# Kernel tuning notes

Measured on AMD Instinct MI355X. Metric: run time of the kernel, lower is better.

## Reference

```python
import jax, jax.numpy as jnp
import numpy as np

DIM = 768
N_HEADS = 12
HEAD_DIM = DIM // N_HEADS
MLP_DIM = 3072
DEPTH = 12
B, N = 16, 512


def setup_inputs() -> dict:
    key = jax.random.key(0)
    ks = jax.random.split(key, 12)
    s = 0.02
    return {
        "x": jax.random.normal(ks[0], (B, N, DIM), dtype=jnp.float32),
        "ln_w": jnp.ones((DIM,), jnp.float32),
        "ln_b": jnp.zeros((DIM,), jnp.float32),
        "wq": jax.random.normal(ks[1], (DIM, DIM), jnp.float32) * s,
        "bq": jnp.zeros((DIM,), jnp.float32),
        "wk": jax.random.normal(ks[2], (DIM, DIM), jnp.float32) * s,
        "bk": jnp.zeros((DIM,), jnp.float32),
        "wv": jax.random.normal(ks[3], (DIM, DIM), jnp.float32) * s,
        "bv": jnp.zeros((DIM,), jnp.float32),
        "w1": jax.random.normal(ks[4], (DIM, MLP_DIM), jnp.float32) * s,
        "b1": jnp.zeros((MLP_DIM,), jnp.float32),
        "w2": jax.random.normal(ks[5], (MLP_DIM, DIM), jnp.float32) * s,
        "b2": jnp.zeros((DIM,), jnp.float32),
    }


def _layernorm(x, w, b):
    mu = jnp.mean(x, axis=-1, keepdims=True)
    var = jnp.var(x, axis=-1, keepdims=True)
    return (x - mu) * jax.lax.rsqrt(var + 1e-5) * w + b


def _mha(x, wq, bq, wk, bk, wv, bv):
    # x: [b, n, dim]; weights stored as [in, out]
    def heads(t):
        return t.reshape(B, N, N_HEADS, HEAD_DIM).transpose(0, 2, 1, 3)  # b h n d
    q = heads(x @ wq + bq)
    k = heads(x @ wk + bk)
    v = heads(x @ wv + bv)
    scores = jnp.einsum('bhqd,bhkd->bhqk', q, k) / np.sqrt(HEAD_DIM).astype(np.float32)
    attn = jax.nn.softmax(scores, axis=-1)
    o = jnp.einsum('bhqk,bhkd->bhqd', attn, v)
    return o.transpose(0, 2, 1, 3).reshape(B, N, DIM)


def reference(x, ln_w, ln_b, wq, bq, wk, bk, wv, bv, w1, b1, w2, b2):
    # Dropout is identity in eval mode. Same weights reused each depth iteration.
    for _ in range(DEPTH):
        x = _mha(_layernorm(x, ln_w, ln_b), wq, bq, wk, bk, wv, bv) + x
        h = _layernorm(x, ln_w, ln_b)
        h = jax.nn.gelu(h @ w1 + b1, approximate=False) @ w2 + b2
        x = h + x
    return x
```

## Files before the change

### kernel.cpp

```cpp
#include <hip/hip_runtime.h>

typedef __bf16 bf16x8 __attribute__((ext_vector_type(8)));
typedef float f32x4 __attribute__((ext_vector_type(4)));
typedef unsigned short ushort8_t __attribute__((ext_vector_type(8)));
typedef unsigned short ushort4_t __attribute__((ext_vector_type(4)));

#define MFMA16(a, b, c) __builtin_amdgcn_mfma_f32_16x16x32_bf16((a), (b), (c), 0, 0, 0)

#define GLOAD16(gp, lp)                                                        \
  __builtin_amdgcn_global_load_lds(                                            \
      (__attribute__((address_space(1))) void*)(gp),                           \
      (__attribute__((address_space(3))) void*)(lp), 16, 0, 0)

#define WAITVM(N) asm volatile("s_waitcnt vmcnt(" #N ")" ::: "memory")
#define SCHEDFENCE __builtin_amdgcn_sched_barrier(0)

__device__ __forceinline__ unsigned short f2bf(float f) {
  unsigned u = __builtin_bit_cast(unsigned, f);
  return (unsigned short)((u + 0x7FFFu + ((u >> 16) & 1u)) >> 16);
}


__global__ __launch_bounds__(256) void transpose_f2b_tiled(
    const float* __restrict__ src, unsigned short* __restrict__ dst,
    int Kdim, int Ndim) {
  const long u = (long)blockIdx.x * 256 + threadIdx.x;
  const long total = ((long)Kdim * Ndim) >> 3;
  if (u >= total) return;
  const int kt32 = Kdim >> 5;
  const long tile = u >> 6;
  const int t8 = (int)(u & 63);
  const int chunk = t8 >> 4, rowlow = t8 & 15;
  const int n = (int)(tile / kt32) * 16 + rowlow;
  const int k0 = (int)(tile % kt32) * 32 + chunk * 8;
  ushort8_t o;
#pragma unroll
  for (int e = 0; e < 8; e++) o[e] = f2bf(src[(long)(k0 + e) * Ndim + n]);
  *(ushort8_t*)(dst + (u << 3)) = o;
}

__global__ __launch_bounds__(256) void ln_kernel(
    const float* __restrict__ x, const float* __restrict__ gw,
    const float* __restrict__ gb, unsigned short* __restrict__ h) {
  const int row = blockIdx.x * 4 + (threadIdx.x >> 6);
  const int l = threadIdx.x & 63;
  const float* xr = x + (long)row * 768;
  f32x4 va[3];
#pragma unroll
  for (int i = 0; i < 3; i++) va[i] = *(const f32x4*)(xr + i * 256 + l * 4);
  float s = 0.f, ss = 0.f;
#pragma unroll
  for (int i = 0; i < 3; i++)
#pragma unroll
    for (int j = 0; j < 4; j++) {
      float t = va[i][j];
      s += t;
      ss += t * t;
    }
#pragma unroll
  for (int off = 1; off < 64; off <<= 1) {
    s += __shfl_xor(s, off, 64);
    ss += __shfl_xor(ss, off, 64);
  }
  const float mu = s * (1.f / 768.f);
  const float var = ss * (1.f / 768.f) - mu * mu;
  const float inv = rsqrtf(var + 1e-5f);
  const long tb = ((long)(row >> 4) * 24) << 9;
  const int rlow = (row & 15) * 8;
  const int coff = ((l >> 1) & 3) * 128 + rlow + (l & 1) * 4;
#pragma unroll
  for (int i = 0; i < 3; i++) {
    f32x4 wv = *(const f32x4*)(gw + i * 256 + l * 4);
    f32x4 bv = *(const f32x4*)(gb + i * 256 + l * 4);
    ushort4_t o;
#pragma unroll
    for (int j = 0; j < 4; j++) o[j] = f2bf((va[i][j] - mu) * inv * wv[j] + bv[j]);
    const long addr = tb + ((long)(i * 8 + (l >> 3)) << 9) + coff;
    *(ushort4_t*)(h + addr) = o;
  }
}

enum { EPI_QKV = 0, EPI_GELU = 1, EPI_RES = 2 };

template <int EPI>
__global__ __launch_bounds__(512) void gemm256p(
    const unsigned short* __restrict__ A, const unsigned short* __restrict__ BT,
    int K, const float* __restrict__ bb0, unsigned short* __restrict__ o0) {
  __shared__ unsigned short As[2][2][8192];
  __shared__ unsigned short Bs[2][2][8192];
  const int tid = threadIdx.x;
  const int w = tid >> 6, l = tid & 63;
  const int lr = l & 15, lg = l >> 4;
  const int wr = w >> 2, wc = w & 3;

  const int nx = gridDim.x;
  const int nwg = nx * gridDim.y;
  int wg = blockIdx.y * nx + blockIdx.x;
  {
    const int qq = nwg >> 3, rr = nwg & 7;
    const int xcd = wg & 7, idx = wg >> 3;
    wg = (xcd < rr ? xcd * (qq + 1) : rr * (qq + 1) + (xcd - rr) * qq) + idx;
  }
  const int bx = wg % nx, by = wg / nx;
  const int m0 = by * 256, n0 = bx * 256;

  const int nk32 = K >> 5;
  const long abase = (long)(m0 >> 4) * nk32;
  const long bbase = (long)(n0 >> 4) * nk32;

  auto stage = [&](int t) {
    const int slot = t & 1;
#pragma unroll
    for (int kk = 0; kk < 2; kk++) {
      const int pk = t * 2 + kk;
      GLOAD16(A + ((abase + (long)w * nk32 + pk) << 9) + l * 8,
              &As[slot][kk][w * 512 + l * 8]);
      GLOAD16(A + ((abase + (long)(w + 8) * nk32 + pk) << 9) + l * 8,
              &As[slot][kk][(w + 8) * 512 + l * 8]);
      GLOAD16(BT + ((bbase + (long)w * nk32 + pk) << 9) + l * 8,
              &Bs[slot][kk][w * 512 + l * 8]);
      GLOAD16(BT + ((bbase + (long)(w + 8) * nk32 + pk) << 9) + l * 8,
              &Bs[slot][kk][(w + 8) * 512 + l * 8]);
    }
  };

  f32x4 acc[8][4] = {};
  const int nk = K >> 6;
  stage(0);
  stage(1);
  for (int t = 0; t < nk; ++t) {
    const int slot = t & 1;
    if (t + 1 < nk) { WAITVM(8); } else { WAITVM(0); }
    SCHEDFENCE;
    __builtin_amdgcn_s_barrier();
    SCHEDFENCE;
#pragma unroll
    for (int kk = 0; kk < 2; kk++) {
      bf16x8 a[8], b[4];
#pragma unroll
      for (int i = 0; i < 8; i++)
        a[i] = *(const bf16x8*)(&As[slot][kk][(wr * 8 + i) * 512 + l * 8]);
#pragma unroll
      for (int j = 0; j < 4; j++)
        b[j] = *(const bf16x8*)(&Bs[slot][kk][(wc * 4 + j) * 512 + l * 8]);
      __builtin_amdgcn_s_setprio(1);
#pragma unroll
      for (int i = 0; i < 8; i++)
#pragma unroll
        for (int j = 0; j < 4; j++) acc[i][j] = MFMA16(a[i], b[j], acc[i][j]);
      __builtin_amdgcn_s_setprio(0);
    }
    SCHEDFENCE;
    __builtin_amdgcn_s_barrier();
    SCHEDFENCE;
    if (t + 2 < nk) stage(t + 2);
  }

#pragma unroll
  for (int fm = 0; fm < 8; fm++) {
    const int r = m0 + wr * 128 + fm * 16 + lg * 4;
#pragma unroll
    for (int fn = 0; fn < 4; fn++) {
      const int c = n0 + wc * 64 + fn * 16 + lr;
      const float bv = bb0[c];
      const long cpart = ((long)(c >> 5) << 9) + ((c >> 3) & 3) * 128 + (c & 7);
#pragma unroll
      for (int q = 0; q < 4; q++) {
        const int row = r + q;
        float v = acc[fm][fn][q] + bv;
        const float u = v * (0.7978845608f + 0.0356774081f * v * v);
        const float g = v / (1.0f + __expf(-2.0f * u));
        o0[(((long)(row >> 4) * 96) << 9) + cpart + (row & 15) * 8] = f2bf(g);
      }
    }
  }
}

template <int EPI, int MREP>
__global__ __launch_bounds__(256) void gemm_bt(
    const unsigned short* __restrict__ A, const unsigned short* __restrict__ BT,
    int K, const float* __restrict__ bb0, const float* __restrict__ bb1,
    const float* __restrict__ bb2, unsigned short* __restrict__ o0,
    unsigned short* __restrict__ o1, unsigned short* __restrict__ o2,
    const float* oFin, float* oFout) {
  constexpr int BM = MREP * 32;
  constexpr int AG = BM / 16;
  __shared__ unsigned short As[2][2][AG * 512];
  __shared__ unsigned short Bs[2][2][8 * 512];
  const int tid = threadIdx.x;
  const int w = tid >> 6, l = tid & 63;
  const int lr = l & 15, lg = l >> 4;
  const int wr = w >> 1, wc = w & 1;

  const int nx = gridDim.x;
  const int nwg = nx * gridDim.y;
  int wg = blockIdx.y * nx + blockIdx.x;
  {
    const int qq = nwg >> 3, rr = nwg & 7;
    const int xcd = wg & 7, idx = wg >> 3;
    wg = (xcd < rr ? xcd * (qq + 1) : rr * (qq + 1) + (xcd - rr) * qq) + idx;
  }
  const int bx = wg % nx, by = wg / nx;
  const int m0 = by * BM, n0 = bx * 128;

  const int nk32 = K >> 5;
  const long abase = (long)(m0 >> 4) * nk32;
  const long bbase = (long)(n0 >> 4) * nk32;

  auto stage = [&](int buf, int kt) {
#pragma unroll
    for (int kk = 0; kk < 2; kk++) {
      const int pk = kt * 2 + kk;
#pragma unroll
      for (int t = 0; t < AG / 4; t++) {
        const int g = w + t * 4;
        GLOAD16(A + ((abase + (long)g * nk32 + pk) << 9) + l * 8,
                &As[buf][kk][g * 512 + l * 8]);
      }
#pragma unroll
      for (int t = 0; t < 2; t++) {
        const int g = w + t * 4;
        GLOAD16(BT + ((bbase + (long)g * nk32 + pk) << 9) + l * 8,
                &Bs[buf][kk][g * 512 + l * 8]);
      }
    }
  };

  f32x4 acc[MREP][4] = {};
  const int nk = K >> 6;
  stage(0, 0);
  for (int kt = 0; kt < nk; ++kt) {
    const int cur = kt & 1;
    __syncthreads();
    if (kt + 1 < nk) stage(cur ^ 1, kt + 1);
#pragma unroll
    for (int kk = 0; kk < 2; kk++) {
      bf16x8 a[MREP], b[4];
#pragma unroll
      for (int i = 0; i < MREP; i++)
        a[i] = *(const bf16x8*)(&As[cur][kk][(wr * MREP + i) * 512 + l * 8]);
#pragma unroll
      for (int j = 0; j < 4; j++)
        b[j] = *(const bf16x8*)(&Bs[cur][kk][(wc * 4 + j) * 512 + l * 8]);
      __builtin_amdgcn_s_setprio(1);
#pragma unroll
      for (int i = 0; i < MREP; i++)
#pragma unroll
        for (int j = 0; j < 4; j++) acc[i][j] = MFMA16(a[i], b[j], acc[i][j]);
      __builtin_amdgcn_s_setprio(0);
    }
  }

  if (EPI == EPI_QKV) {
    const int whichq = n0 / 768;
    const int cc0 = n0 - whichq * 768;
    const float* bias = whichq == 0 ? bb0 : whichq == 1 ? bb1 : bb2;
    if (whichq < 2) {
      unsigned short* dst = whichq == 0 ? o0 : o1;
#pragma unroll
      for (int i = 0; i < MREP; i++) {
        const int r = m0 + wr * MREP * 16 + i * 16 + lg * 4;
#pragma unroll
        for (int j = 0; j < 4; j++) {
          const int ccol = cc0 + wc * 64 + j * 16 + lr;
          const int hd = ccol >> 6, d = ccol & 63;
          const float bv = bias[ccol];
#pragma unroll
          for (int q = 0; q < 4; q++) {
            const int row = r + q;
            const int bidx = row >> 9, n = row & 511;
            const long addr = ((long)(bidx * 12 + hd) * 512 + n) * 64 + d;
            dst[addr] = f2bf(acc[i][j][q] + bv);
          }
        }
      }
    } else {
#pragma unroll
      for (int i = 0; i < MREP; i++) {
        const int r = m0 + wr * MREP * 16 + i * 16 + lg * 4;
        const int bidx = r >> 9, nb = r & 511;
#pragma unroll
        for (int j = 0; j < 4; j++) {
          const int ccol = cc0 + wc * 64 + j * 16 + lr;
          const int hd = ccol >> 6, d = ccol & 63;
          const float bv = bias[ccol];
          ushort4_t pk;
#pragma unroll
          for (int q = 0; q < 4; q++) pk[q] = f2bf(acc[i][j][q] + bv);
          *(ushort4_t*)(&o2[((long)(bidx * 12 + hd) * 64 + d) * 512 + nb]) = pk;
        }
      }
    }
  } else if (EPI == EPI_GELU) {
#pragma unroll
    for (int i = 0; i < MREP; i++) {
      const int r = m0 + wr * MREP * 16 + i * 16 + lg * 4;
#pragma unroll
      for (int j = 0; j < 4; j++) {
        const int c = n0 + wc * 64 + j * 16 + lr;
        const float bv = bb0[c];
        const long cpart = ((long)(c >> 5) << 9) + ((c >> 3) & 3) * 128 + (c & 7);
#pragma unroll
        for (int q = 0; q < 4; q++) {
          const int row = r + q;
          float v = acc[i][j][q] + bv;
          const float u = v * (0.7978845608f + 0.0356774081f * v * v);
          const float g = v / (1.0f + __expf(-2.0f * u));
          o0[(((long)(row >> 4) * 96) << 9) + cpart + (row & 15) * 8] = f2bf(g);
        }
      }
    }
  } else {
#pragma unroll
    for (int i = 0; i < MREP; i++) {
      const int r = m0 + wr * MREP * 16 + i * 16 + lg * 4;
#pragma unroll
      for (int j = 0; j < 4; j++) {
        const int c = n0 + wc * 64 + j * 16 + lr;
        const float bv = bb0[c];
#pragma unroll
        for (int q = 0; q < 4; q++) {
          const long addr = (long)(r + q) * 768 + c;
          oFout[addr] = acc[i][j][q] + bv + oFin[addr];
        }
      }
    }
  }
}

__global__ __launch_bounds__(256) void attn_kernel(
    const unsigned short* __restrict__ qg, const unsigned short* __restrict__ kg,
    const unsigned short* __restrict__ vtg, float* __restrict__ x) {
  __shared__ unsigned short Sh[128 * 64];
  __shared__ unsigned short Ks[2][64 * 64];
  __shared__ unsigned short Vt[2][64 * 64];
  const int qt = blockIdx.x, h = blockIdx.y, b = blockIdx.z;
  const int bh = b * 12 + h;
  const int tid = threadIdx.x, w = tid >> 6, l = tid & 63;
  const int lr = l & 15, lg = l >> 4;
  const int fchunk = ((l & 7) ^ ((l >> 3) & 7)) * 8;
  const int rk = lr & 7;

  const unsigned short* qbase =
      qg + ((long)bh * 512 + qt * 128 + w * 32 + (l >> 3)) * 64 + fchunk;
  unsigned short* shW = &Sh[w * 2048 + l * 8];
#pragma unroll
  for (int cc = 0; cc < 4; cc++) GLOAD16(qbase + cc * 8 * 64, shW + cc * 512);

  const unsigned short* kbase =
      kg + ((long)bh * 512 + w * 16 + (l >> 3)) * 64 + fchunk;
  const unsigned short* vbase =
      vtg + ((long)bh * 64 + w * 16 + (l >> 3)) * 512 + fchunk;
  unsigned short* KsW = &Ks[0][w * 1024 + l * 8];
  unsigned short* VtW = &Vt[0][w * 1024 + l * 8];

  auto stageKV = [&](int buf, int kt) {
#pragma unroll
    for (int cc = 0; cc < 2; cc++) {
      GLOAD16(kbase + (kt * 64 + cc * 8) * 64, KsW + buf * 4096 + cc * 512);
      GLOAD16(vbase + cc * 8 * 512 + kt * 64, VtW + buf * 4096 + cc * 512);
    }
  };
  stageKV(0, 0);
  __syncthreads();

  bf16x8 qa[2][2];
#pragma unroll
  for (int mi = 0; mi < 2; mi++)
#pragma unroll
    for (int ds = 0; ds < 2; ds++) {
      qa[mi][ds] = *(const bf16x8*)(&Sh[(w * 32 + mi * 16 + lr) * 64 +
                                        ((ds * 4 + lg) ^ rk) * 8]);
#pragma unroll
      for (int e = 0; e < 8; e++)
        qa[mi][ds][e] = (__bf16)(0.125f * (float)qa[mi][ds][e]);
    }

  unsigned short* Pw = &Sh[w * 2048];
  float lsum[8] = {};
  f32x4 o[2][4] = {};

  for (int kt = 0; kt < 8; ++kt) {
    const int cur = kt & 1;
    if (kt < 7) stageKV(cur ^ 1, kt + 1);

    f32x4 s[2][4] = {};
#pragma unroll
    for (int ds = 0; ds < 2; ++ds) {
      bf16x8 kb[4];
#pragma unroll
      for (int nj = 0; nj < 4; nj++)
        kb[nj] = *(const bf16x8*)(&Ks[cur][(nj * 16 + lr) * 64 +
                                           ((ds * 4 + lg) ^ rk) * 8]);
#pragma unroll
      for (int mi = 0; mi < 2; mi++)
#pragma unroll
        for (int nj = 0; nj < 4; nj++) s[mi][nj] = MFMA16(qa[mi][ds], kb[nj], s[mi][nj]);
    }

#pragma unroll
    for (int mi = 0; mi < 2; mi++)
#pragma unroll
      for (int nj = 0; nj < 4; nj++) {
        const int cL = nj * 2 + (lr >> 3);
#pragma unroll
        for (int q = 0; q < 4; q++) {
          const int row = mi * 16 + lg * 4 + q;
          const float p = __expf(s[mi][nj][q]);
          lsum[mi * 4 + q] += p;
          Pw[row * 64 + ((cL ^ (row & 7)) * 8) + (lr & 7)] = f2bf(p);
        }
      }

#pragma unroll
    for (int ks = 0; ks < 2; ++ks) {
      bf16x8 pa[2], vb[4];
#pragma unroll
      for (int mi = 0; mi < 2; mi++)
        pa[mi] = *(const bf16x8*)(&Pw[(mi * 16 + lr) * 64 +
                                      ((ks * 4 + lg) ^ rk) * 8]);
#pragma unroll
      for (int dj = 0; dj < 4; dj++)
        vb[dj] = *(const bf16x8*)(&Vt[cur][(dj * 16 + lr) * 64 +
                                           ((ks * 4 + lg) ^ rk) * 8]);
#pragma unroll
      for (int mi = 0; mi < 2; mi++)
#pragma unroll
        for (int dj = 0; dj < 4; dj++) o[mi][dj] = MFMA16(pa[mi], vb[dj], o[mi][dj]);
    }
    __syncthreads();
  }

#pragma unroll
  for (int i = 0; i < 8; i++) {
#pragma unroll
    for (int off = 1; off < 16; off <<= 1) lsum[i] += __shfl_xor(lsum[i], off, 64);
  }

#pragma unroll
  for (int mi = 0; mi < 2; mi++) {
#pragma unroll
    for (int q = 0; q < 4; q++) {
      const int n = qt * 128 + w * 32 + mi * 16 + lg * 4 + q;
      const float inv = 1.0f / lsum[mi * 4 + q];
      const long base = ((long)(b * 512 + n)) * 768 + h * 64;
#pragma unroll
      for (int dj = 0; dj < 4; dj++) {
        const long a = base + dj * 16 + lr;
        x[a] = x[a] + o[mi][dj][q] * inv;
      }
    }
  }
}

extern "C" void kernel_launch(void* const* d_in, const int* in_sizes, int n_in,
                              void* d_out, int out_size, void* d_ws,
                              size_t ws_size, hipStream_t stream) {
  const float* x_in = (const float*)d_in[0];
  const float* ln_w = (const float*)d_in[1];
  const float* ln_b = (const float*)d_in[2];
  const float* wq = (const float*)d_in[3];
  const float* bq = (const float*)d_in[4];
  const float* wk = (const float*)d_in[5];
  const float* bk = (const float*)d_in[6];
  const float* wv = (const float*)d_in[7];
  const float* bv = (const float*)d_in[8];
  const float* w1 = (const float*)d_in[9];
  const float* b1 = (const float*)d_in[10];
  const float* w2 = (const float*)d_in[11];
  const float* b2 = (const float*)d_in[12];

  char* p = (char*)d_ws;
  float* xw = (float*)p;            p += 8192L * 768 * 4;
  unsigned short* hbuf = (unsigned short*)p;  p += 8192L * 768 * 2;
  unsigned short* wqkvT = (unsigned short*)p; p += 2304L * 768 * 2;
  unsigned short* w1T = (unsigned short*)p;   p += 3072L * 768 * 2;
  unsigned short* w2T = (unsigned short*)p;   p += 768L * 3072 * 2;
  unsigned short* qb = (unsigned short*)p;
  unsigned short* kb = qb + 6291456L;
  unsigned short* vt = kb + 6291456L;
  unsigned short* gbuf = qb;

  hipMemcpyAsync(xw, x_in, 8192L * 768 * 4, hipMemcpyDeviceToDevice, stream);

  transpose_f2b_tiled<<<(768 * 768 / 8 + 255) / 256, 256, 0, stream>>>(
      wq, wqkvT, 768, 768);
  transpose_f2b_tiled<<<(768 * 768 / 8 + 255) / 256, 256, 0, stream>>>(
      wk, wqkvT + 768L * 768, 768, 768);
  transpose_f2b_tiled<<<(768 * 768 / 8 + 255) / 256, 256, 0, stream>>>(
      wv, wqkvT + 2L * 768 * 768, 768, 768);
  transpose_f2b_tiled<<<(768 * 3072 / 8 + 255) / 256, 256, 0, stream>>>(
      w1, w1T, 768, 3072);
  transpose_f2b_tiled<<<(768 * 3072 / 8 + 255) / 256, 256, 0, stream>>>(
      w2, w2T, 3072, 768);

  for (int layer = 0; layer < 12; ++layer) {
    ln_kernel<<<2048, 256, 0, stream>>>(xw, ln_w, ln_b, hbuf);
    gemm_bt<EPI_QKV, 4><<<dim3(18, 64), 256, 0, stream>>>(
        hbuf, wqkvT, 768, bq, bk, bv, qb, kb, vt, nullptr, nullptr);
    attn_kernel<<<dim3(4, 12, 16), 256, 0, stream>>>(qb, kb, vt, xw);
    ln_kernel<<<2048, 256, 0, stream>>>(xw, ln_w, ln_b, hbuf);
    gemm256p<EPI_GELU><<<dim3(12, 32), 512, 0, stream>>>(
        hbuf, w1T, 768, b1, gbuf);
    gemm_bt<EPI_RES, 2><<<dim3(6, 128), 256, 0, stream>>>(
        gbuf, w2T, 3072, b2, nullptr, nullptr, nullptr, nullptr, nullptr, xw,
        layer == 11 ? (float*)d_out : xw);
  }
}
```

Before: 2.596 ms.

## Split MLP-up GEMM into four quarter-tile phases with finer-grained LDS staging

Rewrites the 256x256 GELU GEMM so each 64-wide K step is processed as four quadrant sub-phases over A and B half-tiles. LDS is reorganised into four slots holding half-tiles, and global-to-LDS loads for the next halves are issued between the phases. This interleaves memory traffic with MFMA work and reduces register pressure from fragment loads (4 A fragments instead of 8). The cost is four barriers per K step instead of two, plus a more intricate slot-reuse schedule that must avoid overwrite races.

```diff
diff --git a/kernel.cpp b/kernel.cpp
--- a/kernel.cpp
+++ b/kernel.cpp
@@ -13,6 +13,7 @@
       (__attribute__((address_space(3))) void*)(lp), 16, 0, 0)
 
 #define WAITVM(N) asm volatile("s_waitcnt vmcnt(" #N ")" ::: "memory")
+#define WAITLGKM asm volatile("s_waitcnt lgkmcnt(0)" ::: "memory")
 #define SCHEDFENCE __builtin_amdgcn_sched_barrier(0)
 
 __device__ __forceinline__ unsigned short f2bf(float f) {
@@ -82,12 +83,11 @@
 
 enum { EPI_QKV = 0, EPI_GELU = 1, EPI_RES = 2 };
 
-template <int EPI>
-__global__ __launch_bounds__(512) void gemm256p(
+__global__ __launch_bounds__(512) void gemm256f(
     const unsigned short* __restrict__ A, const unsigned short* __restrict__ BT,
     int K, const float* __restrict__ bb0, unsigned short* __restrict__ o0) {
-  __shared__ unsigned short As[2][2][8192];
-  __shared__ unsigned short Bs[2][2][8192];
+  __shared__ unsigned short Asl[4][16 * 512];
+  __shared__ unsigned short Bsl[4][16 * 512];
   const int tid = threadIdx.x;
   const int w = tid >> 6, l = tid & 63;
   const int lr = l & 15, lg = l >> 4;
@@ -108,52 +108,111 @@
   const long abase = (long)(m0 >> 4) * nk32;
   const long bbase = (long)(n0 >> 4) * nk32;
 
-  auto stage = [&](int t) {
-    const int slot = t & 1;
-#pragma unroll
-    for (int kk = 0; kk < 2; kk++) {
-      const int pk = t * 2 + kk;
-      GLOAD16(A + ((abase + (long)w * nk32 + pk) << 9) + l * 8,
-              &As[slot][kk][w * 512 + l * 8]);
-      GLOAD16(A + ((abase + (long)(w + 8) * nk32 + pk) << 9) + l * 8,
-              &As[slot][kk][(w + 8) * 512 + l * 8]);
-      GLOAD16(BT + ((bbase + (long)w * nk32 + pk) << 9) + l * 8,
-              &Bs[slot][kk][w * 512 + l * 8]);
-      GLOAD16(BT + ((bbase + (long)(w + 8) * nk32 + pk) << 9) + l * 8,
-              &Bs[slot][kk][(w + 8) * 512 + l * 8]);
-    }
+  auto stageA = [&](int t, int mh) {
+    const int slot = (2 * t + mh) & 3;
+    const int G = (w >> 2) * 8 + mh * 4 + (w & 3);
+    const int loff = ((w >> 2) * 8 + (w & 3) * 2) * 512;
+#pragma unroll
+    for (int kk = 0; kk < 2; kk++)
+      GLOAD16(A + ((abase + (long)G * nk32 + t * 2 + kk) << 9) + l * 8,
+              &Asl[slot][loff + kk * 512 + l * 8]);
+  };
+  auto stageB = [&](int t, int nh) {
+    const int slot = (2 * t + nh) & 3;
+    const int G = (w >> 1) * 4 + nh * 2 + (w & 1);
+    const int loff = (((w >> 1) * 2 + (w & 1)) * 2) * 512;
+#pragma unroll
+    for (int kk = 0; kk < 2; kk++)
+      GLOAD16(BT + ((bbase + (long)G * nk32 + t * 2 + kk) << 9) + l * 8,
+              &Bsl[slot][loff + kk * 512 + l * 8]);
   };
 
   f32x4 acc[8][4] = {};
   const int nk = K >> 6;
-  stage(0);
-  stage(1);
+
+  stageA(0, 0); stageB(0, 0); stageB(0, 1); stageA(0, 1);
+  stageA(1, 0); stageB(1, 0); stageB(1, 1);
+
   for (int t = 0; t < nk; ++t) {
-    const int slot = t & 1;
-    if (t + 1 < nk) { WAITVM(8); } else { WAITVM(0); }
+    const int sA0 = (2 * t) & 3, sA1 = (2 * t + 1) & 3;
+    if (t < nk - 1) { WAITVM(6); } else { WAITVM(0); }
     SCHEDFENCE;
     __builtin_amdgcn_s_barrier();
     SCHEDFENCE;
-#pragma unroll
-    for (int kk = 0; kk < 2; kk++) {
-      bf16x8 a[8], b[4];
-#pragma unroll
-      for (int i = 0; i < 8; i++)
-        a[i] = *(const bf16x8*)(&As[slot][kk][(wr * 8 + i) * 512 + l * 8]);
-#pragma unroll
-      for (int j = 0; j < 4; j++)
-        b[j] = *(const bf16x8*)(&Bs[slot][kk][(wc * 4 + j) * 512 + l * 8]);
-      __builtin_amdgcn_s_setprio(1);
-#pragma unroll
-      for (int i = 0; i < 8; i++)
-#pragma unroll
-        for (int j = 0; j < 4; j++) acc[i][j] = MFMA16(a[i], b[j], acc[i][j]);
-      __builtin_amdgcn_s_setprio(0);
-    }
+
+    bf16x8 a[4][2], b0[2][2], b1[2][2];
+
+#pragma unroll
+    for (int f = 0; f < 4; f++)
+#pragma unroll
+      for (int kk = 0; kk < 2; kk++)
+        a[f][kk] = *(const bf16x8*)&Asl[sA0][((wr * 4 + f) * 2 + kk) * 512 + l * 8];
+#pragma unroll
+    for (int g2 = 0; g2 < 2; g2++)
+#pragma unroll
+      for (int kk = 0; kk < 2; kk++)
+        b0[g2][kk] = *(const bf16x8*)&Bsl[sA0][((wc * 2 + g2) * 2 + kk) * 512 + l * 8];
+    if (t + 1 < nk) stageA(t + 1, 1);
+    WAITLGKM; SCHEDFENCE;
+    __builtin_amdgcn_s_barrier(); SCHEDFENCE;
+    __builtin_amdgcn_s_setprio(1);
+#pragma unroll
+    for (int f = 0; f < 4; f++)
+#pragma unroll
+      for (int g2 = 0; g2 < 2; g2++)
+#pragma unroll
+        for (int kk = 0; kk < 2; kk++)
+          acc[f][g2] = MFMA16(a[f][kk], b0[g2][kk], acc[f][g2]);
+    __builtin_amdgcn_s_setprio(0);
+
+#pragma unroll
+    for (int g2 = 0; g2 < 2; g2++)
+#pragma unroll
+      for (int kk = 0; kk < 2; kk++)
+        b1[g2][kk] = *(const bf16x8*)&Bsl[sA1][((wc * 2 + g2) * 2 + kk) * 512 + l * 8];
+    if (t + 2 < nk) stageA(t + 2, 0);
+    WAITLGKM; SCHEDFENCE;
+    __builtin_amdgcn_s_barrier(); SCHEDFENCE;
+    __builtin_amdgcn_s_setprio(1);
+#pragma unroll
+    for (int f = 0; f < 4; f++)
+#pragma unroll
+      for (int g2 = 0; g2 < 2; g2++)
+#pragma unroll
+        for (int kk = 0; kk < 2; kk++)
+          acc[f][2 + g2] = MFMA16(a[f][kk], b1[g2][kk], acc[f][2 + g2]);
+    __builtin_amdgcn_s_setprio(0);
+
+#pragma unroll
+    for (int f = 0; f < 4; f++)
+#pragma unroll
+      for (int kk = 0; kk < 2; kk++)
+        a[f][kk] = *(const bf16x8*)&Asl[sA1][((wr * 4 + f) * 2 + kk) * 512 + l * 8];
+    if (t + 2 < nk) stageB(t + 2, 0);
+    WAITLGKM; SCHEDFENCE;
+    __builtin_amdgcn_s_barrier(); SCHEDFENCE;
+    __builtin_amdgcn_s_setprio(1);
+#pragma unroll
+    for (int f = 0; f < 4; f++)
+#pragma unroll
+      for (int g2 = 0; g2 < 2; g2++)
+#pragma unroll
+        for (int kk = 0; kk < 2; kk++)
+          acc[4 + f][2 + g2] = MFMA16(a[f][kk], b1[g2][kk], acc[4 + f][2 + g2]);
+    __builtin_amdgcn_s_setprio(0);
+
+    if (t + 2 < nk) stageB(t + 2, 1);
     SCHEDFENCE;
-    __builtin_amdgcn_s_barrier();
-    SCHEDFENCE;
-    if (t + 2 < nk) stage(t + 2);
+    __builtin_amdgcn_s_barrier(); SCHEDFENCE;
+    __builtin_amdgcn_s_setprio(1);
+#pragma unroll
+    for (int f = 0; f < 4; f++)
+#pragma unroll
+      for (int g2 = 0; g2 < 2; g2++)
+#pragma unroll
+        for (int kk = 0; kk < 2; kk++)
+          acc[4 + f][g2] = MFMA16(a[f][kk], b0[g2][kk], acc[4 + f][g2]);
+    __builtin_amdgcn_s_setprio(0);
   }
 
 #pragma unroll
@@ -500,8 +559,7 @@
         hbuf, wqkvT, 768, bq, bk, bv, qb, kb, vt, nullptr, nullptr);
     attn_kernel<<<dim3(4, 12, 16), 256, 0, stream>>>(qb, kb, vt, xw);
     ln_kernel<<<2048, 256, 0, stream>>>(xw, ln_w, ln_b, hbuf);
-    gemm256p<EPI_GELU><<<dim3(12, 32), 512, 0, stream>>>(
-        hbuf, w1T, 768, b1, gbuf);
+    gemm256f<<<dim3(12, 32), 512, 0, stream>>>(hbuf, w1T, 768, b1, gbuf);
     gemm_bt<EPI_RES, 2><<<dim3(6, 128), 256, 0, stream>>>(
         gbuf, w2T, 3072, b2, nullptr, nullptr, nullptr, nullptr, nullptr, xw,
         layer == 11 ? (float*)d_out : xw);
```

New measurement: 2.544 ms. 2.0% less time.
